# Kernel optimization log

Measured on AMD Instinct MI355X. Metric: run time of the kernel, lower is better.

The kernel has to match this reference:

```python
import jax, jax.numpy as jnp
import numpy as np

B, T, IN, H, OUT, HOR = 512, 720, 6, 128, 3, 360


def _cell(xin, h, c, Wih, Whh, bih, bhh):
    # PyTorch LSTM gate order: i, f, g, o
    g = xin @ Wih.T + h @ Whh.T + bih + bhh
    i, f, gg, o = jnp.split(g, 4, axis=-1)
    c = jax.nn.sigmoid(f) * c + jax.nn.sigmoid(i) * jnp.tanh(gg)
    h = jax.nn.sigmoid(o) * jnp.tanh(c)
    return h, c


def _run_layer(x, Wih, Whh, bih, bhh, reverse):
    xs = x[:, ::-1] if reverse else x
    # hoist input projection out of the scan: (B,T,4H)
    pre = jnp.einsum('bti,gi->btg', xs, Wih) + bih + bhh
    h0 = jnp.zeros((x.shape[0], Whh.shape[1]), x.dtype)

    def step(carry, gt):
        h, c = carry
        g = gt + h @ Whh.T
        i, f, gg, o = jnp.split(g, 4, axis=-1)
        c = jax.nn.sigmoid(f) * c + jax.nn.sigmoid(i) * jnp.tanh(gg)
        h = jax.nn.sigmoid(o) * jnp.tanh(c)
        return (h, c), h

    (hT, cT), ys = jax.lax.scan(step, (h0, h0), jnp.swapaxes(pre, 0, 1))
    ys = jnp.swapaxes(ys, 0, 1)
    if reverse:
        ys = ys[:, ::-1]
    return ys, hT, cT


def reference(x, e0f_Wih, e0f_Whh, e0f_bih, e0f_bhh, e0b_Wih, e0b_Whh, e0b_bih, e0b_bhh,
              e1f_Wih, e1f_Whh, e1f_bih, e1f_bhh, e1b_Wih, e1b_Whh, e1b_bih, e1b_bhh,
              brh_W, brh_b, brc_W, brc_b,
              d0_Wih, d0_Whh, d0_bih, d0_bhh, d1_Wih, d1_Whh, d1_bih, d1_bhh,
              out_W, out_b, start_token):
    b = x.shape[0]
    # bidirectional encoder, layer 0 (input_dim -> H per direction)
    y0f, h0f, c0f = _run_layer(x, e0f_Wih, e0f_Whh, e0f_bih, e0f_bhh, False)
    y0b, h0b, c0b = _run_layer(x, e0b_Wih, e0b_Whh, e0b_bih, e0b_bhh, True)
    y0 = jnp.concatenate([y0f, y0b], axis=-1)  # (B,T,2H)
    # layer 1 (2H -> H per direction); dropout inactive in eval
    _, h1f, c1f = _run_layer(y0, e1f_Wih, e1f_Whh, e1f_bih, e1f_bhh, False)
    _, h1b, c1b = _run_layer(y0, e1b_Wih, e1b_Whh, e1b_bih, e1b_bhh, True)
    # (num_layers, B, 2H): cat fwd/bwd final states per layer
    h_enc = jnp.stack([jnp.concatenate([h0f, h0b], -1), jnp.concatenate([h1f, h1b], -1)])
    c_enc = jnp.stack([jnp.concatenate([c0f, c0b], -1), jnp.concatenate([c1f, c1b], -1)])
    h_dec = h_enc @ brh_W.T + brh_b  # (2,B,H)
    c_dec = c_enc @ brc_W.T + brc_b
    xin0 = jnp.broadcast_to(start_token[0, 0], (b, start_token.shape[-1]))  # (B,3)

    def dec_step(carry, _):
        h0, c0, h1, c1, xin = carry
        h0, c0 = _cell(xin, h0, c0, d0_Wih, d0_Whh, d0_bih, d0_bhh)
        h1, c1 = _cell(h0, h1, c1, d1_Wih, d1_Whh, d1_bih, d1_bhh)
        pred = h1 @ out_W.T + out_b
        return (h0, c0, h1, c1, pred), pred

    carry0 = (h_dec[0], c_dec[0], h_dec[1], c_dec[1], xin0)
    _, preds = jax.lax.scan(dec_step, carry0, None, length=HOR)  # (HOR,B,3)
    return jnp.swapaxes(preds, 0, 1)  # (B,HOR,3)


def setup_inputs() -> dict:
    ks = iter(jax.random.split(jax.random.key(0), 40))

    def p(shape, s=0.05):
        return jax.random.normal(next(ks), shape, dtype=jnp.float32) * s

    d = {"x": jax.random.normal(next(ks), (B, T, IN), dtype=jnp.float32)}
    for name, ind in (("e0f", IN), ("e0b", IN), ("e1f", 2 * H), ("e1b", 2 * H)):
        d[name + "_Wih"] = p((4 * H, ind))
        d[name + "_Whh"] = p((4 * H, H))
        d[name + "_bih"] = p((4 * H,))
        d[name + "_bhh"] = p((4 * H,))
    d["brh_W"] = p((H, 2 * H)); d["brh_b"] = p((H,))
    d["brc_W"] = p((H, 2 * H)); d["brc_b"] = p((H,))
    for name, ind in (("d0", OUT), ("d1", H)):
        d[name + "_Wih"] = p((4 * H, ind))
        d[name + "_Whh"] = p((4 * H, H))
        d[name + "_bih"] = p((4 * H,))
        d[name + "_bhh"] = p((4 * H,))
    d["out_W"] = p((OUT, H)); d["out_b"] = p((OUT,))
    d["start_token"] = p((1, 1, OUT), 0.01)
    return d
```

## Files before the change

### kernel.cpp

```cpp
#include <hip/hip_runtime.h>

typedef __attribute__((ext_vector_type(8))) short bf16x8;
typedef __attribute__((ext_vector_type(4))) float f32x4;

#define MFMA16(a,b,c) __builtin_amdgcn_mfma_f32_16x16x32_bf16((a),(b),(c),0,0,0)

#define T_SEQ  720
#define NB     512
#define HD     128
#define GD     512
#define BT     16
#define HP     136
#define HP0    168
#define YP     264
#define WLP    72
#define HORZ   360

__device__ __forceinline__ float bf2f_(unsigned short u){
  union { unsigned int i; float f; } v; v.i = ((unsigned int)u) << 16; return v.f;
}
__device__ __forceinline__ unsigned short f2bf(float f){
  union { float f; unsigned int i; } v; v.f = f;
  unsigned int r = v.i + 0x7fffu + ((v.i >> 16) & 1u);
  return (unsigned short)(r >> 16);
}
__device__ __forceinline__ float rcp_(float x){ return __builtin_amdgcn_rcpf(x); }
__device__ __forceinline__ float sigm(float x){ return rcp_(1.f + __expf(-x)); }
__device__ __forceinline__ float tanh_(float x){
  float a = fabsf(x);
  float e = __expf(-2.f * a);
  float t = (1.f - e) * rcp_(1.f + e);
  return x >= 0.f ? t : -t;
}
__device__ __forceinline__ bf16x8 cvt8(const float* p){
  bf16x8 r;
  #pragma unroll
  for (int i = 0; i < 8; ++i) r[i] = (short)f2bf(p[i]);
  return r;
}
__device__ __forceinline__ bf16x8 ldg8(const unsigned short* p){
  return *reinterpret_cast<const bf16x8*>(p);
}

__global__ __launch_bounds__(512, 2)
void enc_layer0_kernel(const float* __restrict__ x,
                       const float* __restrict__ WihF, const float* __restrict__ WhhF,
                       const float* __restrict__ bihF, const float* __restrict__ bhhF,
                       const float* __restrict__ WihB, const float* __restrict__ WhhB,
                       const float* __restrict__ bihB, const float* __restrict__ bhhB,
                       unsigned short* __restrict__ y0,
                       float* __restrict__ ench, float* __restrict__ encc)
{
  __shared__ __align__(16) unsigned short h_buf[BT * HP0];
  const int tid  = threadIdx.x;
  const int lane = tid & 63;
  const int w    = tid >> 6;
  const int l15  = lane & 15;
  const int q    = lane >> 4;
  const int dir  = blockIdx.x >> 5;
  const int bbase = (blockIdx.x & 31) * BT;

  const float* Wih = dir ? WihB : WihF;
  const float* Whh = dir ? WhhB : WhhF;
  const float* bih = dir ? bihB : bihF;
  const float* bhh = dir ? bhhB : bhhF;

  bf16x8 bw[4][5];
  float  bias[4];
  #pragma unroll
  for (int g = 0; g < 4; ++g) {
    const int n = g * 128 + w * 16 + l15;
    #pragma unroll
    for (int kt = 0; kt < 4; ++kt)
      bw[g][kt] = cvt8(Whh + n * HD + kt * 32 + q * 8);
    bf16x8 f;
    #pragma unroll
    for (int j = 0; j < 8; ++j) {
      const int kk = q * 8 + j;
      float wv = 0.f;
      if (kk < 6)                wv = Wih[n * 6 + kk];
      else if (kk < 12)          wv = Wih[n * 6 + (kk - 6)];
      f[j] = (short)f2bf(wv);
    }
    bw[g][4] = f;
    bias[g] = bih[n] + bhh[n];
  }

  float cst[4] = {0.f, 0.f, 0.f, 0.f};
  for (int i = tid; i < BT * HP0; i += 512) h_buf[i] = 0;
  __syncthreads();
  if (tid < 96) {
    const int r = tid / 6, k = tid % 6;
    const int t0 = dir ? (T_SEQ - 1) : 0;
    const float v = x[((size_t)(bbase + r) * T_SEQ + t0) * 6 + k];
    const unsigned short hi = f2bf(v);
    const float lo = v - bf2f_(hi);
    h_buf[r * HP0 + 128 + k] = hi;
    h_buf[r * HP0 + 134 + k] = f2bf(lo);
  }
  __syncthreads();

  for (int s = 0; s < T_SEQ; ++s) {
    const int t = dir ? (T_SEQ - 1 - s) : s;

    float xv = 0.f; int xr_ = 0, xk_ = 0;
    const bool xl = (tid < 96) && (s + 1 < T_SEQ);
    if (xl) {
      const int tn = dir ? (T_SEQ - 2 - s) : (s + 1);
      xr_ = tid / 6; xk_ = tid % 6;
      xv = x[((size_t)(bbase + xr_) * T_SEQ + tn) * 6 + xk_];
    }

    f32x4 acc[4];
    #pragma unroll
    for (int g = 0; g < 4; ++g) {
      acc[g][0] = bias[g]; acc[g][1] = bias[g];
      acc[g][2] = bias[g]; acc[g][3] = bias[g];
    }
    #pragma unroll
    for (int kt = 0; kt < 5; ++kt) {
      const bf16x8 af = *reinterpret_cast<const bf16x8*>(&h_buf[l15 * HP0 + kt * 32 + q * 8]);
      #pragma unroll
      for (int g = 0; g < 4; ++g) acc[g] = MFMA16(af, bw[g][kt], acc[g]);
    }
    __syncthreads();

    #pragma unroll
    for (int r = 0; r < 4; ++r) {
      const float i_ = acc[0][r], f_ = acc[1][r], g_ = acc[2][r], o_ = acc[3][r];
      const float c_ = sigm(f_) * cst[r] + sigm(i_) * tanh_(g_);
      cst[r] = c_;
      const float h_ = sigm(o_) * tanh_(c_);
      h_buf[(q * 4 + r) * HP0 + w * 16 + l15] = f2bf(h_);
      if (s == T_SEQ - 1) {
        const int b   = bbase + q * 4 + r;
        const int cix = w * 16 + l15;
        ench[(dir * NB + b) * HD + cix] = h_;
        encc[(dir * NB + b) * HD + cix] = c_;
      }
    }
    if (xl) {
      const unsigned short hi = f2bf(xv);
      const float lo = xv - bf2f_(hi);
      h_buf[xr_ * HP0 + 128 + xk_] = hi;
      h_buf[xr_ * HP0 + 134 + xk_] = f2bf(lo);
    }
    __syncthreads();

    if (tid < 256) {
      const int b = tid >> 4, c8 = tid & 15;
      const bf16x8 hv = *reinterpret_cast<const bf16x8*>(&h_buf[b * HP0 + c8 * 8]);
      *reinterpret_cast<bf16x8*>(y0 + ((size_t)(bbase + b) * T_SEQ + t) * 256 + dir * HD + c8 * 8) = hv;
    }
  }
}

__global__ __launch_bounds__(512, 2)
void enc_layer1_kernel(const unsigned short* __restrict__ y0,
                       const float* __restrict__ WihF, const float* __restrict__ WhhF,
                       const float* __restrict__ bihF, const float* __restrict__ bhhF,
                       const float* __restrict__ WihB, const float* __restrict__ WhhB,
                       const float* __restrict__ bihB, const float* __restrict__ bhhB,
                       float* __restrict__ ench, float* __restrict__ encc)
{
  __shared__ __align__(16) unsigned short wlds[GD * WLP];
  __shared__ __align__(16) unsigned short ybuf[2][BT * YP];
  __shared__ __align__(16) unsigned short h_buf[BT * HP];

  const int tid  = threadIdx.x;
  const int lane = tid & 63;
  const int w    = tid >> 6;
  const int l15  = lane & 15;
  const int q    = lane >> 4;
  const int dir  = blockIdx.x >> 5;
  const int bbase = (blockIdx.x & 31) * BT;

  const float* Wih = dir ? WihB : WihF;
  const float* Whh = dir ? WhhB : WhhF;
  const float* bih = dir ? bihB : bihF;
  const float* bhh = dir ? bhhB : bhhF;

  for (int i = tid; i < GD * 8; i += 512) {
    const int n = i >> 3, c8 = i & 7;
    *reinterpret_cast<bf16x8*>(&wlds[n * WLP + c8 * 8]) = cvt8(Wih + n * 256 + c8 * 8);
  }

  bf16x8 bw[4][10];
  float  bias[4];
  int    nofs[4];
  #pragma unroll
  for (int g = 0; g < 4; ++g) {
    const int n = g * 128 + w * 16 + l15;
    nofs[g] = n * WLP;
    #pragma unroll
    for (int kt = 2; kt < 8; ++kt)  bw[g][kt - 2] = cvt8(Wih + n * 256 + kt * 32 + q * 8);
    #pragma unroll
    for (int kt = 8; kt < 12; ++kt) bw[g][kt - 2] = cvt8(Whh + n * HD + (kt - 8) * 32 + q * 8);
    bias[g] = bih[n] + bhh[n];
  }

  float cst[4] = {0.f, 0.f, 0.f, 0.f};
  for (int i = tid; i < BT * HP; i += 512) h_buf[i] = 0;
  {
    const int t0 = dir ? (T_SEQ - 1) : 0;
    const int b = tid >> 5, c8 = tid & 31;
    *reinterpret_cast<bf16x8*>(&ybuf[0][b * YP + c8 * 8]) =
        ldg8(y0 + ((size_t)(bbase + b) * T_SEQ + t0) * 256 + c8 * 8);
  }
  __syncthreads();

  for (int s = 0; s < T_SEQ; ++s) {
    const int cur = s & 1, nxt = cur ^ 1;

    bf16x8 stg;
    const bool has_next = (s + 1 < T_SEQ);
    const int sb = tid >> 5, sc8 = tid & 31;
    if (has_next) {
      const int t2 = dir ? (T_SEQ - 2 - s) : (s + 1);
      stg = ldg8(y0 + ((size_t)(bbase + sb) * T_SEQ + t2) * 256 + sc8 * 8);
    }

    f32x4 acc[4];
    #pragma unroll
    for (int g = 0; g < 4; ++g) {
      acc[g][0] = bias[g]; acc[g][1] = bias[g];
      acc[g][2] = bias[g]; acc[g][3] = bias[g];
    }
    #pragma unroll
    for (int kt = 0; kt < 2; ++kt) {
      const bf16x8 af = *reinterpret_cast<const bf16x8*>(&ybuf[cur][l15 * YP + kt * 32 + q * 8]);
      #pragma unroll
      for (int g = 0; g < 4; ++g) {
        const bf16x8 bl = *reinterpret_cast<const bf16x8*>(&wlds[nofs[g] + kt * 32 + q * 8]);
        acc[g] = MFMA16(af, bl, acc[g]);
      }
    }
    #pragma unroll
    for (int kt = 2; kt < 8; ++kt) {
      const bf16x8 af = *reinterpret_cast<const bf16x8*>(&ybuf[cur][l15 * YP + kt * 32 + q * 8]);
      #pragma unroll
      for (int g = 0; g < 4; ++g) acc[g] = MFMA16(af, bw[g][kt - 2], acc[g]);
    }
    #pragma unroll
    for (int kt = 8; kt < 12; ++kt) {
      const bf16x8 af = *reinterpret_cast<const bf16x8*>(&h_buf[l15 * HP + (kt - 8) * 32 + q * 8]);
      #pragma unroll
      for (int g = 0; g < 4; ++g) acc[g] = MFMA16(af, bw[g][kt - 2], acc[g]);
    }
    __syncthreads();

    #pragma unroll
    for (int r = 0; r < 4; ++r) {
      const float i_ = acc[0][r], f_ = acc[1][r], g_ = acc[2][r], o_ = acc[3][r];
      const float c_ = sigm(f_) * cst[r] + sigm(i_) * tanh_(g_);
      cst[r] = c_;
      const float h_ = sigm(o_) * tanh_(c_);
      h_buf[(q * 4 + r) * HP + w * 16 + l15] = f2bf(h_);
      if (s == T_SEQ - 1) {
        const int b   = bbase + q * 4 + r;
        const int cix = w * 16 + l15;
        ench[(dir * NB + b) * HD + cix] = h_;
        encc[(dir * NB + b) * HD + cix] = c_;
      }
    }
    if (has_next)
      *reinterpret_cast<bf16x8*>(&ybuf[nxt][sb * YP + sc8 * 8]) = stg;
    __syncthreads();
  }
}

__global__ void bridge_kernel(const float* __restrict__ ench0, const float* __restrict__ encc0,
                              const float* __restrict__ ench1, const float* __restrict__ encc1,
                              const float* __restrict__ brhW, const float* __restrict__ brhb,
                              const float* __restrict__ brcW, const float* __restrict__ brcb,
                              float* __restrict__ dech, float* __restrict__ decc)
{
  const int idx = blockIdx.x * 256 + threadIdx.x;
  const int sel = idx >> 17;
  const int l   = (idx >> 16) & 1;
  const int b   = (idx >> 7) & 511;
  const int j   = idx & 127;
  const float* W  = sel ? brcW : brhW;
  const float* bb = sel ? brcb : brhb;
  const float* s0 = sel ? (l ? encc1 : encc0) : (l ? ench1 : ench0);
  float a = bb[j];
  for (int k = 0; k < 128; ++k) a += W[j * 256 + k] * s0[b * 128 + k];
  for (int k = 0; k < 128; ++k) a += W[j * 256 + 128 + k] * s0[(512 + b) * 128 + k];
  float* dst = sel ? decc : dech;
  dst[(l * 512 + b) * 128 + j] = a;
}

__global__ __launch_bounds__(512, 2)
void decoder_kernel(const float* __restrict__ dech, const float* __restrict__ decc,
                    const float* __restrict__ W0ih, const float* __restrict__ W0hh,
                    const float* __restrict__ b0ih, const float* __restrict__ b0hh,
                    const float* __restrict__ W1ih, const float* __restrict__ W1hh,
                    const float* __restrict__ b1ih, const float* __restrict__ b1hh,
                    const float* __restrict__ outW, const float* __restrict__ outb,
                    const float* __restrict__ stok,
                    float* __restrict__ out)
{
  __shared__ __align__(16) unsigned short w0lds[GD * WLP];
  __shared__ __align__(16) unsigned short w1lds[GD * WLP];
  __shared__ __align__(16) unsigned short h0_buf[BT * HP];
  __shared__ __align__(16) unsigned short h1_buf[BT * HP];
  __shared__ __align__(16) float xin_s[BT][4];

  const int tid  = threadIdx.x;
  const int lane = tid & 63;
  const int w    = tid >> 6;
  const int l15  = lane & 15;
  const int q    = lane >> 4;
  const int bbase = blockIdx.x * BT;

  for (int i = tid; i < GD * 8; i += 512) {
    const int n = i >> 3, c8 = i & 7;
    *reinterpret_cast<bf16x8*>(&w0lds[n * WLP + c8 * 8]) = cvt8(W0hh + n * HD + c8 * 8);
    *reinterpret_cast<bf16x8*>(&w1lds[n * WLP + c8 * 8]) = cvt8(W1ih + n * HD + c8 * 8);
  }

  bf16x8 bw0[4][2];
  bf16x8 bw1[4][6];
  float  xw0[4][3], bias0[4], bias1[4];
  int    nofs[4];
  #pragma unroll
  for (int g = 0; g < 4; ++g) {
    const int n = g * 128 + w * 16 + l15;
    nofs[g] = n * WLP;
    #pragma unroll
    for (int kt = 2; kt < 4; ++kt) {
      bw0[g][kt - 2] = cvt8(W0hh + n * HD + kt * 32 + q * 8);
      bw1[g][kt - 2] = cvt8(W1ih + n * HD + kt * 32 + q * 8);
    }
    #pragma unroll
    for (int kt = 4; kt < 8; ++kt)
      bw1[g][kt - 2] = cvt8(W1hh + n * HD + (kt - 4) * 32 + q * 8);
    #pragma unroll
    for (int k = 0; k < 3; ++k) xw0[g][k] = W0ih[n * 3 + k];
    bias0[g] = b0ih[n] + b0hh[n];
    bias1[g] = b1ih[n] + b1hh[n];
  }

  bf16x8 owf[4];
  float outb_s = 0.f;
  {
    bf16x8 z;
    #pragma unroll
    for (int i = 0; i < 8; ++i) z[i] = 0;
    #pragma unroll
    for (int kt = 0; kt < 4; ++kt) owf[kt] = z;
    if (w == 0 && l15 < 3) {
      #pragma unroll
      for (int kt = 0; kt < 4; ++kt) owf[kt] = cvt8(outW + l15 * HD + kt * 32 + q * 8);
      outb_s = outb[l15];
    }
  }

  float c0[4], c1[4];
  #pragma unroll
  for (int r = 0; r < 4; ++r) {
    const int b   = bbase + q * 4 + r;
    const int cix = w * 16 + l15;
    c0[r] = decc[b * HD + cix];
    c1[r] = decc[(NB + b) * HD + cix];
  }
  for (int i = tid; i < BT * HD; i += 512) {
    const int b = i >> 7, cix = i & 127;
    h0_buf[b * HP + cix] = f2bf(dech[(bbase + b) * HD + cix]);
    h1_buf[b * HP + cix] = f2bf(dech[(NB + bbase + b) * HD + cix]);
  }
  if (tid < 64) {
    const int b = tid >> 2, o = tid & 3;
    xin_s[b][o] = (o < 3) ? stok[o] : 0.f;
  }
  __syncthreads();

  for (int s = 0; s < HORZ; ++s) {
    f32x4 acc[4];
    float xr[4][3];
    #pragma unroll
    for (int r = 0; r < 4; ++r) {
      xr[r][0] = xin_s[q * 4 + r][0];
      xr[r][1] = xin_s[q * 4 + r][1];
      xr[r][2] = xin_s[q * 4 + r][2];
    }
    #pragma unroll
    for (int g = 0; g < 4; ++g)
      #pragma unroll
      for (int r = 0; r < 4; ++r)
        acc[g][r] = bias0[g] + xw0[g][0] * xr[r][0] + xw0[g][1] * xr[r][1] + xw0[g][2] * xr[r][2];
    #pragma unroll
    for (int kt = 0; kt < 2; ++kt) {
      const bf16x8 af = *reinterpret_cast<const bf16x8*>(&h0_buf[l15 * HP + kt * 32 + q * 8]);
      #pragma unroll
      for (int g = 0; g < 4; ++g) {
        const bf16x8 bl = *reinterpret_cast<const bf16x8*>(&w0lds[nofs[g] + kt * 32 + q * 8]);
        acc[g] = MFMA16(af, bl, acc[g]);
      }
    }
    #pragma unroll
    for (int kt = 2; kt < 4; ++kt) {
      const bf16x8 af = *reinterpret_cast<const bf16x8*>(&h0_buf[l15 * HP + kt * 32 + q * 8]);
      #pragma unroll
      for (int g = 0; g < 4; ++g) acc[g] = MFMA16(af, bw0[g][kt - 2], acc[g]);
    }
    __syncthreads();
    #pragma unroll
    for (int r = 0; r < 4; ++r) {
      const float i_ = acc[0][r], f_ = acc[1][r], g_ = acc[2][r], o_ = acc[3][r];
      const float c_ = sigm(f_) * c0[r] + sigm(i_) * tanh_(g_);
      c0[r] = c_;
      const float h_ = sigm(o_) * tanh_(c_);
      h0_buf[(q * 4 + r) * HP + w * 16 + l15] = f2bf(h_);
    }
    __syncthreads();

    #pragma unroll
    for (int g = 0; g < 4; ++g) {
      acc[g][0] = bias1[g]; acc[g][1] = bias1[g];
      acc[g][2] = bias1[g]; acc[g][3] = bias1[g];
    }
    #pragma unroll
    for (int kt = 0; kt < 2; ++kt) {
      const bf16x8 af = *reinterpret_cast<const bf16x8*>(&h0_buf[l15 * HP + kt * 32 + q * 8]);
      #pragma unroll
      for (int g = 0; g < 4; ++g) {
        const bf16x8 bl = *reinterpret_cast<const bf16x8*>(&w1lds[nofs[g] + kt * 32 + q * 8]);
        acc[g] = MFMA16(af, bl, acc[g]);
      }
    }
    #pragma unroll
    for (int kt = 2; kt < 4; ++kt) {
      const bf16x8 af = *reinterpret_cast<const bf16x8*>(&h0_buf[l15 * HP + kt * 32 + q * 8]);
      #pragma unroll
      for (int g = 0; g < 4; ++g) acc[g] = MFMA16(af, bw1[g][kt - 2], acc[g]);
    }
    #pragma unroll
    for (int kt = 4; kt < 8; ++kt) {
      const bf16x8 af = *reinterpret_cast<const bf16x8*>(&h1_buf[l15 * HP + (kt - 4) * 32 + q * 8]);
      #pragma unroll
      for (int g = 0; g < 4; ++g) acc[g] = MFMA16(af, bw1[g][kt - 2], acc[g]);
    }
    __syncthreads();
    #pragma unroll
    for (int r = 0; r < 4; ++r) {
      const float i_ = acc[0][r], f_ = acc[1][r], g_ = acc[2][r], o_ = acc[3][r];
      const float c_ = sigm(f_) * c1[r] + sigm(i_) * tanh_(g_);
      c1[r] = c_;
      const float h_ = sigm(o_) * tanh_(c_);
      h1_buf[(q * 4 + r) * HP + w * 16 + l15] = f2bf(h_);
    }
    __syncthreads();

    if (w == 0) {
      f32x4 p = {0.f, 0.f, 0.f, 0.f};
      #pragma unroll
      for (int kt = 0; kt < 4; ++kt) {
        const bf16x8 af = *reinterpret_cast<const bf16x8*>(&h1_buf[l15 * HP + kt * 32 + q * 8]);
        p = MFMA16(af, owf[kt], p);
      }
      if (l15 < 3) {
        #pragma unroll
        for (int r = 0; r < 4; ++r) {
          const float v = p[r] + outb_s;
          const int b = q * 4 + r;
          xin_s[b][l15] = v;
          out[((size_t)(bbase + b) * HORZ + s) * 3 + l15] = v;
        }
      }
    }
    __syncthreads();
  }
}

extern "C" void kernel_launch(void* const* d_in, const int* in_sizes, int n_in,
                              void* d_out, int out_size, void* d_ws, size_t ws_size,
                              hipStream_t stream)
{
  (void)in_sizes; (void)n_in; (void)out_size; (void)ws_size;
  const float* x      = (const float*)d_in[0];
  const float* e0fWih = (const float*)d_in[1];
  const float* e0fWhh = (const float*)d_in[2];
  const float* e0fbih = (const float*)d_in[3];
  const float* e0fbhh = (const float*)d_in[4];
  const float* e0bWih = (const float*)d_in[5];
  const float* e0bWhh = (const float*)d_in[6];
  const float* e0bbih = (const float*)d_in[7];
  const float* e0bbhh = (const float*)d_in[8];
  const float* e1fWih = (const float*)d_in[9];
  const float* e1fWhh = (const float*)d_in[10];
  const float* e1fbih = (const float*)d_in[11];
  const float* e1fbhh = (const float*)d_in[12];
  const float* e1bWih = (const float*)d_in[13];
  const float* e1bWhh = (const float*)d_in[14];
  const float* e1bbih = (const float*)d_in[15];
  const float* e1bbhh = (const float*)d_in[16];
  const float* brhW   = (const float*)d_in[17];
  const float* brhb   = (const float*)d_in[18];
  const float* brcW   = (const float*)d_in[19];
  const float* brcb   = (const float*)d_in[20];
  const float* d0Wih  = (const float*)d_in[21];
  const float* d0Whh  = (const float*)d_in[22];
  const float* d0bih  = (const float*)d_in[23];
  const float* d0bhh  = (const float*)d_in[24];
  const float* d1Wih  = (const float*)d_in[25];
  const float* d1Whh  = (const float*)d_in[26];
  const float* d1bih  = (const float*)d_in[27];
  const float* d1bhh  = (const float*)d_in[28];
  const float* outW   = (const float*)d_in[29];
  const float* outb   = (const float*)d_in[30];
  const float* stok   = (const float*)d_in[31];

  char* ws = (char*)d_ws;
  unsigned short* y0 = (unsigned short*)ws;
  size_t off = (size_t)NB * T_SEQ * 256 * sizeof(unsigned short);
  const size_t blk = (size_t)2 * NB * HD * sizeof(float);
  float* ench0 = (float*)(ws + off); off += blk;
  float* encc0 = (float*)(ws + off); off += blk;
  float* ench1 = (float*)(ws + off); off += blk;
  float* encc1 = (float*)(ws + off); off += blk;
  float* dech  = (float*)(ws + off); off += blk;
  float* decc  = (float*)(ws + off); off += blk;

  enc_layer0_kernel<<<dim3(64), dim3(512), 0, stream>>>(
      x, e0fWih, e0fWhh, e0fbih, e0fbhh, e0bWih, e0bWhh, e0bbih, e0bbhh,
      y0, ench0, encc0);
  enc_layer1_kernel<<<dim3(64), dim3(512), 0, stream>>>(
      y0, e1fWih, e1fWhh, e1fbih, e1fbhh, e1bWih, e1bWhh, e1bbih, e1bbhh,
      ench1, encc1);
  bridge_kernel<<<dim3(1024), dim3(256), 0, stream>>>(
      ench0, encc0, ench1, encc1, brhW, brhb, brcW, brcb, dech, decc);
  decoder_kernel<<<dim3(32), dim3(512), 0, stream>>>(
      dech, decc, d0Wih, d0Whh, d0bih, d0bhh, d1Wih, d1Whh, d1bih, d1bhh,
      outW, outb, stok, (float*)d_out);
}
```

Measured before the change: 3.257 ms.

## Double-buffer recurrent state to drop barriers; async LDS loads with swizzle

Hidden-state buffers in all three recurrent kernels become ping-pong buffers, which removes one __syncthreads per step in the encoders and two per step in the decoder. Layer 1 now stages the next y0 timestep straight into LDS with global_load_lds and an XOR swizzle in place of padded rows. Layer 0 moves its y0 store and x prefetch one step ahead. The decoder has every wave compute the output projection redundantly and passes the feedback input through shuffles instead of LDS. In exchange it costs more LDS, redundant MFMA work, and relies on the async LDS load finishing by the next barrier.

Measured after the change: 3.036 ms. -6.8%, faster.

```diff
diff --git a/kernel.cpp b/kernel.cpp
--- a/kernel.cpp
+++ b/kernel.cpp
@@ -12,8 +12,8 @@
 #define BT     16
 #define HP     136
 #define HP0    168
-#define YP     264
-#define WLP    72
+#define YT     256
+#define WLP    68
 #define HORZ   360
 
 __device__ __forceinline__ float bf2f_(unsigned short u){
@@ -38,8 +38,10 @@
   for (int i = 0; i < 8; ++i) r[i] = (short)f2bf(p[i]);
   return r;
 }
-__device__ __forceinline__ bf16x8 ldg8(const unsigned short* p){
-  return *reinterpret_cast<const bf16x8*>(p);
+__device__ __forceinline__ void gl_lds16(const unsigned short* g, unsigned short* l){
+  __builtin_amdgcn_global_load_lds(
+      (const __attribute__((address_space(1))) void*)(g),
+      (__attribute__((address_space(3))) void*)(l), 16, 0, 0);
 }
 
 __global__ __launch_bounds__(512, 2)
@@ -51,7 +53,7 @@
                        unsigned short* __restrict__ y0,
                        float* __restrict__ ench, float* __restrict__ encc)
 {
-  __shared__ __align__(16) unsigned short h_buf[BT * HP0];
+  __shared__ __align__(16) unsigned short h_buf[2][BT * HP0];
   const int tid  = threadIdx.x;
   const int lane = tid & 63;
   const int w    = tid >> 6;
@@ -78,38 +80,42 @@
     for (int j = 0; j < 8; ++j) {
       const int kk = q * 8 + j;
       float wv = 0.f;
-      if (kk < 6)                wv = Wih[n * 6 + kk];
-      else if (kk < 12)          wv = Wih[n * 6 + (kk - 6)];
+      if (kk < 6)       wv = Wih[n * 6 + kk];
+      else if (kk < 12) wv = Wih[n * 6 + (kk - 6)];
       f[j] = (short)f2bf(wv);
     }
     bw[g][4] = f;
     bias[g] = bih[n] + bhh[n];
   }
 
+  int t = dir ? (T_SEQ - 1) : 0;
+  const int dt = dir ? -1 : 1;
+  const int xr_ = tid / 6, xk_ = tid % 6;
+
   float cst[4] = {0.f, 0.f, 0.f, 0.f};
-  for (int i = tid; i < BT * HP0; i += 512) h_buf[i] = 0;
+  for (int i = tid; i < 2 * BT * HP0; i += 512) (&h_buf[0][0])[i] = 0;
   __syncthreads();
+  float xv_cur = 0.f;
   if (tid < 96) {
-    const int r = tid / 6, k = tid % 6;
-    const int t0 = dir ? (T_SEQ - 1) : 0;
-    const float v = x[((size_t)(bbase + r) * T_SEQ + t0) * 6 + k];
-    const unsigned short hi = f2bf(v);
-    const float lo = v - bf2f_(hi);
-    h_buf[r * HP0 + 128 + k] = hi;
-    h_buf[r * HP0 + 134 + k] = f2bf(lo);
+    const float v0 = x[((size_t)(bbase + xr_) * T_SEQ + t) * 6 + xk_];
+    const unsigned short hi = f2bf(v0);
+    h_buf[0][xr_ * HP0 + 128 + xk_] = hi;
+    h_buf[0][xr_ * HP0 + 134 + xk_] = f2bf(v0 - bf2f_(hi));
+    xv_cur = x[((size_t)(bbase + xr_) * T_SEQ + t + dt) * 6 + xk_];
   }
   __syncthreads();
 
-  for (int s = 0; s < T_SEQ; ++s) {
-    const int t = dir ? (T_SEQ - 1 - s) : s;
-
-    float xv = 0.f; int xr_ = 0, xk_ = 0;
-    const bool xl = (tid < 96) && (s + 1 < T_SEQ);
-    if (xl) {
-      const int tn = dir ? (T_SEQ - 2 - s) : (s + 1);
-      xr_ = tid / 6; xk_ = tid % 6;
-      xv = x[((size_t)(bbase + xr_) * T_SEQ + tn) * 6 + xk_];
-    }
+  for (int s = 0; s < T_SEQ; ++s, t += dt) {
+    const int cur = s & 1, nxt = cur ^ 1;
+
+    if (s > 0 && tid < 256) {
+      const int b = tid >> 4, c8 = tid & 15;
+      const bf16x8 hv = *reinterpret_cast<const bf16x8*>(&h_buf[cur][b * HP0 + c8 * 8]);
+      *reinterpret_cast<bf16x8*>(y0 + ((size_t)(bbase + b) * T_SEQ + (t - dt)) * 256 + dir * HD + c8 * 8) = hv;
+    }
+    float xv_next = 0.f;
+    if (tid < 96 && s + 2 < T_SEQ)
+      xv_next = x[((size_t)(bbase + xr_) * T_SEQ + (t + 2 * dt)) * 6 + xk_];
 
     f32x4 acc[4];
     #pragma unroll
@@ -119,11 +125,10 @@
     }
     #pragma unroll
     for (int kt = 0; kt < 5; ++kt) {
-      const bf16x8 af = *reinterpret_cast<const bf16x8*>(&h_buf[l15 * HP0 + kt * 32 + q * 8]);
+      const bf16x8 af = *reinterpret_cast<const bf16x8*>(&h_buf[cur][l15 * HP0 + kt * 32 + q * 8]);
       #pragma unroll
       for (int g = 0; g < 4; ++g) acc[g] = MFMA16(af, bw[g][kt], acc[g]);
     }
-    __syncthreads();
 
     #pragma unroll
     for (int r = 0; r < 4; ++r) {
@@ -131,7 +136,7 @@
       const float c_ = sigm(f_) * cst[r] + sigm(i_) * tanh_(g_);
       cst[r] = c_;
       const float h_ = sigm(o_) * tanh_(c_);
-      h_buf[(q * 4 + r) * HP0 + w * 16 + l15] = f2bf(h_);
+      h_buf[nxt][(q * 4 + r) * HP0 + w * 16 + l15] = f2bf(h_);
       if (s == T_SEQ - 1) {
         const int b   = bbase + q * 4 + r;
         const int cix = w * 16 + l15;
@@ -139,19 +144,20 @@
         encc[(dir * NB + b) * HD + cix] = c_;
       }
     }
-    if (xl) {
-      const unsigned short hi = f2bf(xv);
-      const float lo = xv - bf2f_(hi);
-      h_buf[xr_ * HP0 + 128 + xk_] = hi;
-      h_buf[xr_ * HP0 + 134 + xk_] = f2bf(lo);
-    }
+    if (tid < 96 && s + 1 < T_SEQ) {
+      const unsigned short hi = f2bf(xv_cur);
+      h_buf[nxt][xr_ * HP0 + 128 + xk_] = hi;
+      h_buf[nxt][xr_ * HP0 + 134 + xk_] = f2bf(xv_cur - bf2f_(hi));
+    }
+    xv_cur = xv_next;
     __syncthreads();
-
-    if (tid < 256) {
-      const int b = tid >> 4, c8 = tid & 15;
-      const bf16x8 hv = *reinterpret_cast<const bf16x8*>(&h_buf[b * HP0 + c8 * 8]);
-      *reinterpret_cast<bf16x8*>(y0 + ((size_t)(bbase + b) * T_SEQ + t) * 256 + dir * HD + c8 * 8) = hv;
-    }
+  }
+  if (tid < 256) {
+    const int cur = T_SEQ & 1;
+    const int b = tid >> 4, c8 = tid & 15;
+    const bf16x8 hv = *reinterpret_cast<const bf16x8*>(&h_buf[cur][b * HP0 + c8 * 8]);
+    const int tl = dir ? 0 : (T_SEQ - 1);
+    *reinterpret_cast<bf16x8*>(y0 + ((size_t)(bbase + b) * T_SEQ + tl) * 256 + dir * HD + c8 * 8) = hv;
   }
 }
 
@@ -164,8 +170,8 @@
                        float* __restrict__ ench, float* __restrict__ encc)
 {
   __shared__ __align__(16) unsigned short wlds[GD * WLP];
-  __shared__ __align__(16) unsigned short ybuf[2][BT * YP];
-  __shared__ __align__(16) unsigned short h_buf[BT * HP];
+  __shared__ __align__(16) unsigned short ybuf[2][BT * YT];
+  __shared__ __align__(16) unsigned short h_buf[2][BT * HP];
 
   const int tid  = threadIdx.x;
   const int lane = tid & 63;
@@ -199,26 +205,26 @@
     bias[g] = bih[n] + bhh[n];
   }
 
+  const int sb   = 2 * w + (lane >> 5);
+  const int cimg = lane & 31;
+  const int sig  = (cimg & 16) | ((cimg & 15) ^ (sb & 15));
+  const size_t grow = (size_t)(bbase + sb) * T_SEQ * 256 + (size_t)sig * 8;
+  unsigned short* ldst0 = &ybuf[0][w * 512];
+  unsigned short* ldst1 = &ybuf[1][w * 512];
+
+  int t = dir ? (T_SEQ - 1) : 0;
+  const int dt = dir ? -1 : 1;
+
   float cst[4] = {0.f, 0.f, 0.f, 0.f};
-  for (int i = tid; i < BT * HP; i += 512) h_buf[i] = 0;
-  {
-    const int t0 = dir ? (T_SEQ - 1) : 0;
-    const int b = tid >> 5, c8 = tid & 31;
-    *reinterpret_cast<bf16x8*>(&ybuf[0][b * YP + c8 * 8]) =
-        ldg8(y0 + ((size_t)(bbase + b) * T_SEQ + t0) * 256 + c8 * 8);
-  }
+  for (int i = tid; i < 2 * BT * HP; i += 512) (&h_buf[0][0])[i] = 0;
+  gl_lds16(y0 + grow + (size_t)t * 256, ldst0);
   __syncthreads();
 
-  for (int s = 0; s < T_SEQ; ++s) {
+  for (int s = 0; s < T_SEQ; ++s, t += dt) {
     const int cur = s & 1, nxt = cur ^ 1;
 
-    bf16x8 stg;
-    const bool has_next = (s + 1 < T_SEQ);
-    const int sb = tid >> 5, sc8 = tid & 31;
-    if (has_next) {
-      const int t2 = dir ? (T_SEQ - 2 - s) : (s + 1);
-      stg = ldg8(y0 + ((size_t)(bbase + sb) * T_SEQ + t2) * 256 + sc8 * 8);
-    }
+    if (s + 1 < T_SEQ)
+      gl_lds16(y0 + grow + (size_t)(t + dt) * 256, cur ? ldst0 : ldst1);
 
     f32x4 acc[4];
     #pragma unroll
@@ -228,7 +234,8 @@
     }
     #pragma unroll
     for (int kt = 0; kt < 2; ++kt) {
-      const bf16x8 af = *reinterpret_cast<const bf16x8*>(&ybuf[cur][l15 * YP + kt * 32 + q * 8]);
+      const int swz = ((kt * 4 + q) & 15) ^ l15;
+      const bf16x8 af = *reinterpret_cast<const bf16x8*>(&ybuf[cur][l15 * YT + swz * 8]);
       #pragma unroll
       for (int g = 0; g < 4; ++g) {
         const bf16x8 bl = *reinterpret_cast<const bf16x8*>(&wlds[nofs[g] + kt * 32 + q * 8]);
@@ -237,17 +244,18 @@
     }
     #pragma unroll
     for (int kt = 2; kt < 8; ++kt) {
-      const bf16x8 af = *reinterpret_cast<const bf16x8*>(&ybuf[cur][l15 * YP + kt * 32 + q * 8]);
+      const int c   = kt * 4 + q;
+      const int swz = (c & 16) | ((c & 15) ^ l15);
+      const bf16x8 af = *reinterpret_cast<const bf16x8*>(&ybuf[cur][l15 * YT + swz * 8]);
       #pragma unroll
       for (int g = 0; g < 4; ++g) acc[g] = MFMA16(af, bw[g][kt - 2], acc[g]);
     }
     #pragma unroll
     for (int kt = 8; kt < 12; ++kt) {
-      const bf16x8 af = *reinterpret_cast<const bf16x8*>(&h_buf[l15 * HP + (kt - 8) * 32 + q * 8]);
+      const bf16x8 af = *reinterpret_cast<const bf16x8*>(&h_buf[cur][l15 * HP + (kt - 8) * 32 + q * 8]);
       #pragma unroll
       for (int g = 0; g < 4; ++g) acc[g] = MFMA16(af, bw[g][kt - 2], acc[g]);
     }
-    __syncthreads();
 
     #pragma unroll
     for (int r = 0; r < 4; ++r) {
@@ -255,7 +263,7 @@
       const float c_ = sigm(f_) * cst[r] + sigm(i_) * tanh_(g_);
       cst[r] = c_;
       const float h_ = sigm(o_) * tanh_(c_);
-      h_buf[(q * 4 + r) * HP + w * 16 + l15] = f2bf(h_);
+      h_buf[nxt][(q * 4 + r) * HP + w * 16 + l15] = f2bf(h_);
       if (s == T_SEQ - 1) {
         const int b   = bbase + q * 4 + r;
         const int cix = w * 16 + l15;
@@ -263,8 +271,6 @@
         encc[(dir * NB + b) * HD + cix] = c_;
       }
     }
-    if (has_next)
-      *reinterpret_cast<bf16x8*>(&ybuf[nxt][sb * YP + sc8 * 8]) = stg;
     __syncthreads();
   }
 }
@@ -302,9 +308,8 @@
 {
   __shared__ __align__(16) unsigned short w0lds[GD * WLP];
   __shared__ __align__(16) unsigned short w1lds[GD * WLP];
-  __shared__ __align__(16) unsigned short h0_buf[BT * HP];
-  __shared__ __align__(16) unsigned short h1_buf[BT * HP];
-  __shared__ __align__(16) float xin_s[BT][4];
+  __shared__ __align__(16) unsigned short h0_buf[2][BT * HP];
+  __shared__ __align__(16) unsigned short h1_buf[2][BT * HP];
 
   const int tid  = threadIdx.x;
   const int lane = tid & 63;
@@ -349,7 +354,7 @@
     for (int i = 0; i < 8; ++i) z[i] = 0;
     #pragma unroll
     for (int kt = 0; kt < 4; ++kt) owf[kt] = z;
-    if (w == 0 && l15 < 3) {
+    if (l15 < 3) {
       #pragma unroll
       for (int kt = 0; kt < 4; ++kt) owf[kt] = cvt8(outW + l15 * HD + kt * 32 + q * 8);
       outb_s = outb[l15];
@@ -366,24 +371,21 @@
   }
   for (int i = tid; i < BT * HD; i += 512) {
     const int b = i >> 7, cix = i & 127;
-    h0_buf[b * HP + cix] = f2bf(dech[(bbase + b) * HD + cix]);
-    h1_buf[b * HP + cix] = f2bf(dech[(NB + bbase + b) * HD + cix]);
-  }
-  if (tid < 64) {
-    const int b = tid >> 2, o = tid & 3;
-    xin_s[b][o] = (o < 3) ? stok[o] : 0.f;
+    h0_buf[0][b * HP + cix] = f2bf(dech[(bbase + b) * HD + cix]);
+    h1_buf[0][b * HP + cix] = f2bf(dech[(NB + bbase + b) * HD + cix]);
+  }
+  float xr[4][3];
+  {
+    const float s0 = stok[0], s1 = stok[1], s2 = stok[2];
+    #pragma unroll
+    for (int r = 0; r < 4; ++r) { xr[r][0] = s0; xr[r][1] = s1; xr[r][2] = s2; }
   }
   __syncthreads();
 
   for (int s = 0; s < HORZ; ++s) {
+    const int cur = s & 1, nxt = cur ^ 1;
+
     f32x4 acc[4];
-    float xr[4][3];
-    #pragma unroll
-    for (int r = 0; r < 4; ++r) {
-      xr[r][0] = xin_s[q * 4 + r][0];
-      xr[r][1] = xin_s[q * 4 + r][1];
-      xr[r][2] = xin_s[q * 4 + r][2];
-    }
     #pragma unroll
     for (int g = 0; g < 4; ++g)
       #pragma unroll
@@ -391,7 +393,7 @@
         acc[g][r] = bias0[g] + xw0[g][0] * xr[r][0] + xw0[g][1] * xr[r][1] + xw0[g][2] * xr[r][2];
     #pragma unroll
     for (int kt = 0; kt < 2; ++kt) {
-      const bf16x8 af = *reinterpret_cast<const bf16x8*>(&h0_buf[l15 * HP + kt * 32 + q * 8]);
+      const bf16x8 af = *reinterpret_cast<const bf16x8*>(&h0_buf[cur][l15 * HP + kt * 32 + q * 8]);
       #pragma unroll
       for (int g = 0; g < 4; ++g) {
         const bf16x8 bl = *reinterpret_cast<const bf16x8*>(&w0lds[nofs[g] + kt * 32 + q * 8]);
@@ -400,18 +402,17 @@
     }
     #pragma unroll
     for (int kt = 2; kt < 4; ++kt) {
-      const bf16x8 af = *reinterpret_cast<const bf16x8*>(&h0_buf[l15 * HP + kt * 32 + q * 8]);
+      const bf16x8 af = *reinterpret_cast<const bf16x8*>(&h0_buf[cur][l15 * HP + kt * 32 + q * 8]);
       #pragma unroll
       for (int g = 0; g < 4; ++g) acc[g] = MFMA16(af, bw0[g][kt - 2], acc[g]);
     }
-    __syncthreads();
     #pragma unroll
     for (int r = 0; r < 4; ++r) {
       const float i_ = acc[0][r], f_ = acc[1][r], g_ = acc[2][r], o_ = acc[3][r];
       const float c_ = sigm(f_) * c0[r] + sigm(i_) * tanh_(g_);
       c0[r] = c_;
       const float h_ = sigm(o_) * tanh_(c_);
-      h0_buf[(q * 4 + r) * HP + w * 16 + l15] = f2bf(h_);
+      h0_buf[nxt][(q * 4 + r) * HP + w * 16 + l15] = f2bf(h_);
     }
     __syncthreads();
 
@@ -422,7 +423,7 @@
     }
     #pragma unroll
     for (int kt = 0; kt < 2; ++kt) {
-      const bf16x8 af = *reinterpret_cast<const bf16x8*>(&h0_buf[l15 * HP + kt * 32 + q * 8]);
+      const bf16x8 af = *reinterpret_cast<const bf16x8*>(&h0_buf[nxt][l15 * HP + kt * 32 + q * 8]);
       #pragma unroll
       for (int g = 0; g < 4; ++g) {
         const bf16x8 bl = *reinterpret_cast<const bf16x8*>(&w1lds[nofs[g] + kt * 32 + q * 8]);
@@ -431,45 +432,45 @@
     }
     #pragma unroll
     for (int kt = 2; kt < 4; ++kt) {
-      const bf16x8 af = *reinterpret_cast<const bf16x8*>(&h0_buf[l15 * HP + kt * 32 + q * 8]);
+      const bf16x8 af = *reinterpret_cast<const bf16x8*>(&h0_buf[nxt][l15 * HP + kt * 32 + q * 8]);
       #pragma unroll
       for (int g = 0; g < 4; ++g) acc[g] = MFMA16(af, bw1[g][kt - 2], acc[g]);
     }
     #pragma unroll
     for (int kt = 4; kt < 8; ++kt) {
-      const bf16x8 af = *reinterpret_cast<const bf16x8*>(&h1_buf[l15 * HP + (kt - 4) * 32 + q * 8]);
+      const bf16x8 af = *reinterpret_cast<const bf16x8*>(&h1_buf[cur][l15 * HP + (kt - 4) * 32 + q * 8]);
       #pragma unroll
       for (int g = 0; g < 4; ++g) acc[g] = MFMA16(af, bw1[g][kt - 2], acc[g]);
     }
-    __syncthreads();
     #pragma unroll
     for (int r = 0; r < 4; ++r) {
       const float i_ = acc[0][r], f_ = acc[1][r], g_ = acc[2][r], o_ = acc[3][r];
       const float c_ = sigm(f_) * c1[r] + sigm(i_) * tanh_(g_);
       c1[r] = c_;
       const float h_ = sigm(o_) * tanh_(c_);
-      h1_buf[(q * 4 + r) * HP + w * 16 + l15] = f2bf(h_);
+      h1_buf[nxt][(q * 4 + r) * HP + w * 16 + l15] = f2bf(h_);
     }
     __syncthreads();
 
-    if (w == 0) {
-      f32x4 p = {0.f, 0.f, 0.f, 0.f};
-      #pragma unroll
-      for (int kt = 0; kt < 4; ++kt) {
-        const bf16x8 af = *reinterpret_cast<const bf16x8*>(&h1_buf[l15 * HP + kt * 32 + q * 8]);
-        p = MFMA16(af, owf[kt], p);
-      }
-      if (l15 < 3) {
-        #pragma unroll
-        for (int r = 0; r < 4; ++r) {
-          const float v = p[r] + outb_s;
-          const int b = q * 4 + r;
-          xin_s[b][l15] = v;
-          out[((size_t)(bbase + b) * HORZ + s) * 3 + l15] = v;
-        }
-      }
-    }
-    __syncthreads();
+    f32x4 p = {0.f, 0.f, 0.f, 0.f};
+    #pragma unroll
+    for (int kt = 0; kt < 4; ++kt) {
+      const bf16x8 af = *reinterpret_cast<const bf16x8*>(&h1_buf[nxt][l15 * HP + kt * 32 + q * 8]);
+      p = MFMA16(af, owf[kt], p);
+    }
+    float pb[4];
+    #pragma unroll
+    for (int r = 0; r < 4; ++r) pb[r] = p[r] + outb_s;
+    if (w == 0 && l15 < 3) {
+      #pragma unroll
+      for (int r = 0; r < 4; ++r)
+        out[((size_t)(bbase + q * 4 + r) * HORZ + s) * 3 + l15] = pb[r];
+    }
+    #pragma unroll
+    for (int r = 0; r < 4; ++r)
+      #pragma unroll
+      for (int c = 0; c < 3; ++c)
+        xr[r][c] = __shfl(pb[r], (q << 4) + c, 64);
   }
 }
 
```
